# Kernel optimization log

Hardware: AMD Instinct MI355X
Metric: run time of the kernel (lower is better)

Reference implementation:

```python
import jax, jax.numpy as jnp
import numpy as np

P, R, S = 512, 128, 128   # num_proposal, ref_length, src_length
K = 3                      # top-k per row/column
THRESHOLD = 0.05
MUTUAL = False
CONDITIONAL = True


def setup_inputs() -> dict:
    key = jax.random.key(0)
    k1, k2, k3, k4 = jax.random.split(key, 4)
    return {
        "matching_score_map": jax.random.normal(k1, (P, R, S), dtype=jnp.float32),
        "ref_knn_masks": jax.random.bernoulli(k2, 0.9, (P, R)),
        "src_knn_masks": jax.random.bernoulli(k3, 0.9, (P, S)),
        "node_corr_scores": jax.random.uniform(k4, (P,), dtype=jnp.float32),
    }


def reference(matching_score_map, ref_knn_masks, src_knn_masks, node_corr_scores):
    # matching_score_map: [P, R, S] log-scores -> exp, as in torch forward
    m = jnp.exp(matching_score_map)
    p, r, s = m.shape
    # corr_mask_map = ref_mask[:, :, None] & src_mask[:, None, :] -> [P, R, S]
    corr_mask_map = jnp.logical_and(ref_knn_masks[:, :, None], src_knn_masks[:, None, :])

    pidx = jnp.arange(p)[:, None, None]

    # top-k along src dim (dim=2), scatter back into a sparse score map
    ref_topk_scores, ref_topk_idx = jax.lax.top_k(m, K)           # [P, R, K]
    ridx = jnp.arange(r)[None, :, None]
    ref_score_map = jnp.zeros_like(m).at[pidx, ridx, ref_topk_idx].set(ref_topk_scores)

    # top-k along ref dim (dim=1): transpose, top_k, scatter, transpose back
    mt = jnp.swapaxes(m, 1, 2)                                    # [P, S, R]
    src_topk_scores, src_topk_idx = jax.lax.top_k(mt, K)          # [P, S, K]
    sidx = jnp.arange(s)[None, :, None]
    src_score_map = jnp.swapaxes(
        jnp.zeros_like(mt).at[pidx, sidx, src_topk_idx].set(src_topk_scores), 1, 2
    )

    ref_corr_map = jnp.logical_and(ref_score_map > THRESHOLD, corr_mask_map)
    src_corr_map = jnp.logical_and(src_score_map > THRESHOLD, corr_mask_map)

    score_map = (ref_score_map + src_score_map) * 0.5
    if MUTUAL:
        corr_map = jnp.logical_and(ref_corr_map, src_corr_map)
    else:
        corr_map = jnp.logical_or(ref_corr_map, src_corr_map)
    if CONDITIONAL:
        score_map = score_map * node_corr_scores[:, None, None]
    return score_map, corr_map
```

## Files before the change

kernel.cpp:

```cpp
#include <hip/hip_runtime.h>


typedef float vf4 __attribute__((ext_vector_type(4)));
typedef int   vi4 __attribute__((ext_vector_type(4)));

constexpr int NP = 512;
constexpr int NR = 128;
constexpr int NS = 128;
constexpr int RS = NR * NS;
constexpr float THRESHOLD = 0.05f;
constexpr float NEG_INF = -3.4e38f;

__device__ __forceinline__ void top3_insert(float v, float& m0, float& m1, float& m2) {
    float n1 = __builtin_amdgcn_fmed3f(v, m0, m1);
    float n2 = __builtin_amdgcn_fmed3f(v, m1, m2);
    m0 = fmaxf(m0, v);
    m1 = n1; m2 = n2;
}

__device__ __forceinline__ void shfl_merge3(int d, float& m0, float& m1, float& m2) {
    float o0 = __shfl_xor(m0, d);
    float o1 = __shfl_xor(m1, d);
    float o2 = __shfl_xor(m2, d);
    top3_insert(o0, m0, m1, m2);
    top3_insert(o1, m0, m1, m2);
    top3_insert(o2, m0, m1, m2);
}

__global__ __launch_bounds__(512, 2) void fused_kernel(
    const float* __restrict__ in,
    const int*   __restrict__ rmask,
    const int*   __restrict__ smask,
    const float* __restrict__ ncs,
    float*       __restrict__ out)
{
    __shared__ vf4   tile4[RS / 4];
    __shared__ float thirds[NS];
    const int p   = blockIdx.x;
    const int t   = threadIdx.x;
    const int row = t >> 2;
    const int q   = t & 3;

    const vf4* b4 = (const vf4*)(in + (size_t)p * RS);

    vf4 x[8];
    float r0 = NEG_INF, r1 = NEG_INF, r2 = NEG_INF;
    #pragma unroll
    for (int j = 0; j < 8; ++j) {
        int c4 = q + 4 * j;
        x[j] = b4[row * 32 + c4];
        tile4[row * 32 + (c4 ^ (row & 31))] = x[j];
        top3_insert(x[j].x, r0, r1, r2);
        top3_insert(x[j].y, r0, r1, r2);
        top3_insert(x[j].z, r0, r1, r2);
        top3_insert(x[j].w, r0, r1, r2);
    }
    shfl_merge3(1, r0, r1, r2);
    shfl_merge3(2, r0, r1, r2);
    const float tr = r2;
    __syncthreads();

    {
        const int col = t >> 2, seg = t & 3;
        const int c4c = col >> 2, cw = col & 3;
        const float* tf = (const float*)tile4;
        float c0 = NEG_INF, c1 = NEG_INF, c2 = NEG_INF;
        #pragma unroll 8
        for (int i = 0; i < 32; ++i) {
            int r = 4 * seg + (i & 3) + 16 * (i >> 2);
            top3_insert(tf[r * 128 + ((c4c ^ (r & 31)) << 2) + cw], c0, c1, c2);
        }
        shfl_merge3(1, c0, c1, c2);
        shfl_merge3(2, c0, c1, c2);
        if (seg == 0) thirds[col] = c2;
    }
    __syncthreads();

    const float halfnc = 0.5f * ncs[p];
    const float mrf    = (rmask[p * NR + row] != 0) ? 1.0f : 0.0f;
    vf4* sc4 = (vf4*)(out + (size_t)p * RS);
    vf4* co4 = (vf4*)(out + (size_t)(NP + p) * RS);
    const vi4* sm4 = (const vi4*)(smask + (size_t)p * NS);
    const vf4* th4 = (const vf4*)thirds;

    #pragma unroll
    for (int j = 0; j < 8; ++j) {
        int c4 = q + 4 * j;
        vf4 tc = th4[c4];
        vi4 ms = sm4[c4];
        vf4 v  = x[j];
        vf4 sc, co;

        {   float e = __expf(v.x);
            float w = ((v.x >= tr) ? halfnc : 0.f) + ((v.x >= tc.x) ? halfnc : 0.f);
            sc.x = e * w;
            float mk = (ms.x != 0) ? mrf : 0.f;
            co.x = (e > THRESHOLD && w > 0.f) ? mk : 0.f; }
        {   float e = __expf(v.y);
            float w = ((v.y >= tr) ? halfnc : 0.f) + ((v.y >= tc.y) ? halfnc : 0.f);
            sc.y = e * w;
            float mk = (ms.y != 0) ? mrf : 0.f;
            co.y = (e > THRESHOLD && w > 0.f) ? mk : 0.f; }
        {   float e = __expf(v.z);
            float w = ((v.z >= tr) ? halfnc : 0.f) + ((v.z >= tc.z) ? halfnc : 0.f);
            sc.z = e * w;
            float mk = (ms.z != 0) ? mrf : 0.f;
            co.z = (e > THRESHOLD && w > 0.f) ? mk : 0.f; }
        {   float e = __expf(v.w);
            float w = ((v.w >= tr) ? halfnc : 0.f) + ((v.w >= tc.w) ? halfnc : 0.f);
            sc.w = e * w;
            float mk = (ms.w != 0) ? mrf : 0.f;
            co.w = (e > THRESHOLD && w > 0.f) ? mk : 0.f; }

        sc4[row * 32 + c4] = sc;
        co4[row * 32 + c4] = co;
    }
}

extern "C" void kernel_launch(void* const* d_in, const int* in_sizes, int n_in,
                              void* d_out, int out_size, void* d_ws, size_t ws_size,
                              hipStream_t stream) {
    const float* msm   = (const float*)d_in[0];
    const int*   rmask = (const int*)  d_in[1];
    const int*   smask = (const int*)  d_in[2];
    const float* ncs   = (const float*)d_in[3];
    float* out = (float*)d_out;

    fused_kernel<<<NP, 512, 0, stream>>>(msm, rmask, smask, ncs, out);
}
```

Baseline: 97.13 us.

## Process two proposals per block with async global-to-LDS prefetch of the next tile

Each block now handles two proposals instead of one. Tiles are loaded with global_load_lds straight into a double-buffered, XOR-swizzled shared-memory tile, and the second proposal's tile is prefetched while the first is reduced and written out. This aims to hide global load latency behind compute and output stores, and to skip staging the tile through registers. In exchange the grid is halved to 256 blocks, which lowers parallelism and occupancy, and LDS use doubles.

```diff
diff --git a/kernel.cpp b/kernel.cpp
--- a/kernel.cpp
+++ b/kernel.cpp
@@ -27,6 +27,12 @@
     top3_insert(o2, m0, m1, m2);
 }
 
+__device__ __forceinline__ void async_load16(const float* g, float* l) {
+    __builtin_amdgcn_global_load_lds(
+        (__attribute__((address_space(1))) void*)(g),
+        (__attribute__((address_space(3))) void*)(l), 16, 0, 0);
+}
+
 __global__ __launch_bounds__(512, 2) void fused_kernel(
     const float* __restrict__ in,
     const int*   __restrict__ rmask,
@@ -34,86 +40,122 @@
     const float* __restrict__ ncs,
     float*       __restrict__ out)
 {
-    __shared__ vf4   tile4[RS / 4];
-    __shared__ float thirds[NS];
-    const int p   = blockIdx.x;
-    const int t   = threadIdx.x;
-    const int row = t >> 2;
-    const int q   = t & 3;
+    __shared__ vf4 tile4[2][RS / 4];
+    __shared__ __align__(16) float thirds[2][NS];
 
-    const vf4* b4 = (const vf4*)(in + (size_t)p * RS);
+    const int t    = threadIdx.x;
+    const int wv   = t >> 6;
+    const int lane = t & 63;
+    const int row  = t >> 2;
+    const int q    = t & 3;
+    const int p0   = blockIdx.x * 2;
 
-    vf4 x[8];
-    float r0 = NEG_INF, r1 = NEG_INF, r2 = NEG_INF;
-    #pragma unroll
-    for (int j = 0; j < 8; ++j) {
-        int c4 = q + 4 * j;
-        x[j] = b4[row * 32 + c4];
-        tile4[row * 32 + (c4 ^ (row & 31))] = x[j];
-        top3_insert(x[j].x, r0, r1, r2);
-        top3_insert(x[j].y, r0, r1, r2);
-        top3_insert(x[j].z, r0, r1, r2);
-        top3_insert(x[j].w, r0, r1, r2);
-    }
-    shfl_merge3(1, r0, r1, r2);
-    shfl_merge3(2, r0, r1, r2);
-    const float tr = r2;
-    __syncthreads();
-
-    {
-        const int col = t >> 2, seg = t & 3;
-        const int c4c = col >> 2, cw = col & 3;
-        const float* tf = (const float*)tile4;
-        float c0 = NEG_INF, c1 = NEG_INF, c2 = NEG_INF;
-        #pragma unroll 8
-        for (int i = 0; i < 32; ++i) {
-            int r = 4 * seg + (i & 3) + 16 * (i >> 2);
-            top3_insert(tf[r * 128 + ((c4c ^ (r & 31)) << 2) + cw], c0, c1, c2);
-        }
-        shfl_merge3(1, c0, c1, c2);
-        shfl_merge3(2, c0, c1, c2);
-        if (seg == 0) thirds[col] = c2;
-    }
-    __syncthreads();
-
-    const float halfnc = 0.5f * ncs[p];
-    const float mrf    = (rmask[p * NR + row] != 0) ? 1.0f : 0.0f;
-    vf4* sc4 = (vf4*)(out + (size_t)p * RS);
-    vf4* co4 = (vf4*)(out + (size_t)(NP + p) * RS);
-    const vi4* sm4 = (const vi4*)(smask + (size_t)p * NS);
-    const vf4* th4 = (const vf4*)thirds;
+    const float* src0 = in + (size_t)p0 * RS;
+    const float* src1 = in + (size_t)(p0 + 1) * RS;
 
     #pragma unroll
     for (int j = 0; j < 8; ++j) {
-        int c4 = q + 4 * j;
-        vf4 tc = th4[c4];
-        vi4 ms = sm4[c4];
-        vf4 v  = x[j];
-        vf4 sc, co;
+        int s  = (wv * 8 + j) * 64 + lane;
+        int r  = s >> 5;
+        int c4 = (s & 31) ^ (r & 31);
+        async_load16(src0 + r * 128 + c4 * 4, (float*)&tile4[0][(wv * 8 + j) * 64]);
+    }
+    const float halfnc0 = 0.5f * ncs[p0];
+    const float halfnc1 = 0.5f * ncs[p0 + 1];
+    const float mrf0 = (rmask[p0 * NR + row] != 0) ? 1.0f : 0.0f;
+    const float mrf1 = (rmask[(p0 + 1) * NR + row] != 0) ? 1.0f : 0.0f;
+    __syncthreads();
 
-        {   float e = __expf(v.x);
-            float w = ((v.x >= tr) ? halfnc : 0.f) + ((v.x >= tc.x) ? halfnc : 0.f);
-            sc.x = e * w;
-            float mk = (ms.x != 0) ? mrf : 0.f;
-            co.x = (e > THRESHOLD && w > 0.f) ? mk : 0.f; }
-        {   float e = __expf(v.y);
-            float w = ((v.y >= tr) ? halfnc : 0.f) + ((v.y >= tc.y) ? halfnc : 0.f);
-            sc.y = e * w;
-            float mk = (ms.y != 0) ? mrf : 0.f;
-            co.y = (e > THRESHOLD && w > 0.f) ? mk : 0.f; }
-        {   float e = __expf(v.z);
-            float w = ((v.z >= tr) ? halfnc : 0.f) + ((v.z >= tc.z) ? halfnc : 0.f);
-            sc.z = e * w;
-            float mk = (ms.z != 0) ? mrf : 0.f;
-            co.z = (e > THRESHOLD && w > 0.f) ? mk : 0.f; }
-        {   float e = __expf(v.w);
-            float w = ((v.w >= tr) ? halfnc : 0.f) + ((v.w >= tc.w) ? halfnc : 0.f);
-            sc.w = e * w;
-            float mk = (ms.w != 0) ? mrf : 0.f;
-            co.w = (e > THRESHOLD && w > 0.f) ? mk : 0.f; }
+    #pragma unroll
+    for (int pp = 0; pp < 2; ++pp) {
+        const int p = p0 + pp;
 
-        sc4[row * 32 + c4] = sc;
-        co4[row * 32 + c4] = co;
+        if (pp == 0) {
+            #pragma unroll
+            for (int j = 0; j < 8; ++j) {
+                int s  = (wv * 8 + j) * 64 + lane;
+                int r  = s >> 5;
+                int c4 = (s & 31) ^ (r & 31);
+                async_load16(src1 + r * 128 + c4 * 4,
+                             (float*)&tile4[1][(wv * 8 + j) * 64]);
+            }
+        }
+
+        const vi4* sm4 = (const vi4*)(smask + (size_t)p * NS);
+        vi4 ms[8];
+        #pragma unroll
+        for (int j = 0; j < 8; ++j) ms[j] = sm4[q + 4 * j];
+
+        const vf4* tb = tile4[pp];
+        vf4 x[8];
+        float r0 = NEG_INF, r1 = NEG_INF, r2 = NEG_INF;
+        #pragma unroll
+        for (int j = 0; j < 8; ++j) {
+            int c4 = q + 4 * j;
+            x[j] = tb[row * 32 + (c4 ^ (row & 31))];
+            top3_insert(x[j].x, r0, r1, r2);
+            top3_insert(x[j].y, r0, r1, r2);
+            top3_insert(x[j].z, r0, r1, r2);
+            top3_insert(x[j].w, r0, r1, r2);
+        }
+        shfl_merge3(1, r0, r1, r2);
+        shfl_merge3(2, r0, r1, r2);
+        const float tr = r2;
+
+        {
+            const int col = t >> 2, seg = t & 3;
+            const int c4c = col >> 2, cw = col & 3;
+            const float* tf = (const float*)tb;
+            float c0 = NEG_INF, c1 = NEG_INF, c2 = NEG_INF;
+            #pragma unroll 8
+            for (int i = 0; i < 32; ++i) {
+                int r = 4 * seg + (i & 3) + 16 * (i >> 2);
+                top3_insert(tf[r * 128 + ((c4c ^ (r & 31)) << 2) + cw], c0, c1, c2);
+            }
+            shfl_merge3(1, c0, c1, c2);
+            shfl_merge3(2, c0, c1, c2);
+            if (seg == 0) thirds[pp][col] = c2;
+        }
+        __syncthreads();
+
+        const float halfnc = pp ? halfnc1 : halfnc0;
+        const float mrf    = pp ? mrf1 : mrf0;
+        vf4* sc4 = (vf4*)(out + (size_t)p * RS);
+        vf4* co4 = (vf4*)(out + (size_t)(NP + p) * RS);
+        const vf4* th4 = (const vf4*)thirds[pp];
+
+        #pragma unroll
+        for (int j = 0; j < 8; ++j) {
+            int c4 = q + 4 * j;
+            vf4 tc = th4[c4];
+            vi4 m  = ms[j];
+            vf4 v  = x[j];
+            vf4 sc, co;
+
+            {   float e = __expf(v.x);
+                float w2 = ((v.x >= tr) ? halfnc : 0.f) + ((v.x >= tc.x) ? halfnc : 0.f);
+                sc.x = e * w2;
+                float mk = (m.x != 0) ? mrf : 0.f;
+                co.x = (e > THRESHOLD && w2 > 0.f) ? mk : 0.f; }
+            {   float e = __expf(v.y);
+                float w2 = ((v.y >= tr) ? halfnc : 0.f) + ((v.y >= tc.y) ? halfnc : 0.f);
+                sc.y = e * w2;
+                float mk = (m.y != 0) ? mrf : 0.f;
+                co.y = (e > THRESHOLD && w2 > 0.f) ? mk : 0.f; }
+            {   float e = __expf(v.z);
+                float w2 = ((v.z >= tr) ? halfnc : 0.f) + ((v.z >= tc.z) ? halfnc : 0.f);
+                sc.z = e * w2;
+                float mk = (m.z != 0) ? mrf : 0.f;
+                co.z = (e > THRESHOLD && w2 > 0.f) ? mk : 0.f; }
+            {   float e = __expf(v.w);
+                float w2 = ((v.w >= tr) ? halfnc : 0.f) + ((v.w >= tc.w) ? halfnc : 0.f);
+                sc.w = e * w2;
+                float mk = (m.w != 0) ? mrf : 0.f;
+                co.w = (e > THRESHOLD && w2 > 0.f) ? mk : 0.f; }
+
+            sc4[row * 32 + c4] = sc;
+            co4[row * 32 + c4] = co;
+        }
     }
 }
 
@@ -126,5 +168,5 @@
     const float* ncs   = (const float*)d_in[3];
     float* out = (float*)d_out;
 
-    fused_kernel<<<NP, 512, 0, stream>>>(msm, rmask, smask, ncs, out);
+    fused_kernel<<<NP / 2, 512, 0, stream>>>(msm, rmask, smask, ncs, out);
 }
```

Result: no change. 97.29 us (+0.2%).
